# Kernel tuning notes

Hardware: AMD Instinct MI355X
Metric: run time of the kernel (lower is better)

The kernel has to match this reference:

```python
import jax, jax.numpy as jnp
import numpy as np

HIDDEN = 1024
MOE_INTER = 512
SHARED_INTER = 2048
N_EXPERTS = 32
TOP_K = 6
N_GROUP = 8
TOPK_GROUP = 4
ROUTED_SCALE = 2.5


def setup_inputs() -> dict:
    key = jax.random.key(0)
    ks = jax.random.split(key, 6)
    s = 0.02
    return {
        "hidden_states": jax.random.normal(ks[0], (2, 1024, HIDDEN), jnp.float32),
        "gate_w": jax.random.normal(ks[1], (N_EXPERTS, HIDDEN), jnp.float32) * s,
        "e_bias": jnp.zeros((N_EXPERTS,), jnp.float32),  # e_score_correction_bias (non-trainable)
        "up_w": jax.random.normal(ks[2], (N_EXPERTS, MOE_INTER, HIDDEN), jnp.float32) * s,
        "down_w": jax.random.normal(ks[3], (N_EXPERTS, HIDDEN, MOE_INTER), jnp.float32) * s,
        "shared_up_w": jax.random.normal(ks[4], (SHARED_INTER, HIDDEN), jnp.float32) * s,
        "shared_down_w": jax.random.normal(ks[5], (HIDDEN, SHARED_INTER), jnp.float32) * s,
    }


def _relu2(x):
    # Nemotron-H 'relu2' activation: relu(x)^2
    return jnp.square(jax.nn.relu(x))


def _router(x, gate_w, e_bias):
    # x: [T, H] -> topk_idx [T, K] (int), topk_w [T, K] (fp32)
    T = x.shape[0]
    logits = x.astype(jnp.float32) @ gate_w.astype(jnp.float32).T  # [T, E]
    scores = jax.nn.sigmoid(logits)
    sc = scores + e_bias[None, :]
    # group-limited routing: top-2 sum per group, keep topk_group groups
    g = sc.reshape(T, N_GROUP, N_EXPERTS // N_GROUP)
    group_scores = jax.lax.top_k(g, 2)[0].sum(-1)                  # [T, G]
    group_idx = jax.lax.top_k(group_scores, TOPK_GROUP)[1]         # [T, TG]
    group_mask = jnp.zeros_like(group_scores).at[jnp.arange(T)[:, None], group_idx].set(1.0)
    score_mask = jnp.repeat(group_mask, N_EXPERTS // N_GROUP, axis=1)  # [T, E]
    masked = jnp.where(score_mask > 0, sc, 0.0)
    topk_idx = jax.lax.stop_gradient(jax.lax.top_k(masked, TOP_K)[1])  # torch path is @no_grad
    topk_w = jnp.take_along_axis(scores, topk_idx, axis=1)         # gather from unbiased scores
    topk_w = topk_w / (topk_w.sum(-1, keepdims=True) + 1e-20)      # norm_topk_prob
    topk_w = topk_w * ROUTED_SCALE
    return topk_idx, topk_w


def reference(hidden_states, gate_w, e_bias, up_w, down_w, shared_up_w, shared_down_w):
    B, S, H = hidden_states.shape
    x = hidden_states.reshape(-1, H)  # [T, H]
    T = x.shape[0]
    topk_idx, topk_w = _router(x, gate_w, e_bias)
    # combine weights as dense [T, E] (scatter of top-k weights)
    combine = jnp.zeros((T, N_EXPERTS), topk_w.dtype).at[jnp.arange(T)[:, None], topk_idx].add(topk_w)
    # dense-masked expert compute; weight applied on intermediate (equivalent since
    # down_proj is linear with no bias): out = sum_e w_te * down_e(act(up_e(x)))
    h = _relu2(jnp.einsum('th,eih->tei', x, up_w))   # [T, E, I]
    h = h * combine[:, :, None]
    moe_out = jnp.einsum('tei,ehi->th', h, down_w)   # [T, H]
    shared = _relu2(x @ shared_up_w.T) @ shared_down_w.T
    return (moe_out + shared).reshape(B, S, H)


if __name__ == "__main__":
    out = reference(**setup_inputs())
    print(out.shape, out.dtype)
```

## Files before the change

### kernel.cpp

```cpp
#include <hip/hip_runtime.h>

typedef unsigned short u16;
typedef __bf16 bf16x8 __attribute__((ext_vector_type(8)));
typedef float f32x4 __attribute__((ext_vector_type(4)));
typedef u16 u16x8 __attribute__((ext_vector_type(8)));

#define T_TOK 2048
#define HID   1024
#define NEXP  32
#define IM    512
#define SI    2048
#define TOPK  6
#define PLAN_MAX 160

__device__ __forceinline__ u16 f2bf(float f){
  unsigned u = __float_as_uint(f);
  u += 0x7FFFu + ((u >> 16) & 1u);
  return (u16)(u >> 16);
}

__device__ __forceinline__ void gll16(const void* g, void* l){
  __builtin_amdgcn_global_load_lds((const __attribute__((address_space(1))) void*)g,
                                   (__attribute__((address_space(3))) void*)l, 16, 0, 0);
}

__device__ __forceinline__ u16x8 cvt2(float4 a, float4 b){
  u16x8 o;
  o[0] = f2bf(a.x); o[1] = f2bf(a.y); o[2] = f2bf(a.z); o[3] = f2bf(a.w);
  o[4] = f2bf(b.x); o[5] = f2bf(b.y); o[6] = f2bf(b.z); o[7] = f2bf(b.w);
  return o;
}

__global__ __launch_bounds__(256) void prep_kernel(
    const float* __restrict__ x, const float4* __restrict__ upw, const float4* __restrict__ dnw,
    const float4* __restrict__ supw, const float4* __restrict__ sdnw,
    const float* __restrict__ gate, const float* __restrict__ ebias,
    u16x8* __restrict__ xb, u16x8* __restrict__ upb, u16x8* __restrict__ dnb,
    u16x8* __restrict__ supb, u16x8* __restrict__ sdnb,
    int* __restrict__ ce, float* __restrict__ cw, int* __restrict__ done){
  int blk = blockIdx.x;
  if (blk == 0 && threadIdx.x == 0) *done = 0;
  if (blk >= 512){
    const float4* s; u16x8* d; long i;
    if (blk < 16896){
      i = (long)(blk - 512) * 256 + threadIdx.x;
      if (i < 2097152L){ s = upw; d = upb; }
      else             { s = dnw; d = dnb; i -= 2097152L; }
    } else {
      i = (long)(blk - 16896) * 256 + threadIdx.x;
      if      (i < 262144L){ s = (const float4*)x; d = xb; }
      else if (i < 524288L){ s = supw; d = supb; i -= 262144L; }
      else                 { s = sdnw; d = sdnb; i -= 524288L; }
    }
    float4 a = s[2*i], b = s[2*i+1];
    d[i] = cvt2(a, b);
    return;
  }
  int wave = threadIdx.x >> 6;
  int lane = threadIdx.x & 63;
  int t = blk * 4 + wave;
  int e = lane & 31, half = lane >> 5;
  const float4* xv = (const float4*)(x + (size_t)t * HID);
  const float4* gv = (const float4*)(gate + (size_t)e * HID);
  double d0a = 0, d1a = 0, d2a = 0, d3a = 0;
  for (int i = half * 128; i < half * 128 + 128; i++){
    float4 a = xv[i], b = gv[i];
    d0a += (double)a.x * b.x; d1a += (double)a.y * b.y;
    d2a += (double)a.z * b.z; d3a += (double)a.w * b.w;
  }
  double acc = (d0a + d1a) + (d2a + d3a);
  acc += __shfl_xor(acc, 32);
  double score = 1.0 / (1.0 + exp(-acc));
  double sc = score + (double)ebias[e];
  double o1  = __shfl_xor(sc, 1);
  double hi  = fmax(sc, o1), lo = fmin(sc, o1);
  double ohi = __shfl_xor(hi, 2), olo = __shfl_xor(lo, 2);
  double gs  = (hi >= ohi) ? hi + fmax(lo, ohi) : ohi + fmax(olo, hi);
  int g = e >> 2;
  int rank = 0;
#pragma unroll
  for (int j = 0; j < 8; j++){
    double gj = __shfl(gs, j * 4);
    if (gj > gs || (gj == gs && j < g)) rank++;
  }
  double cur = (rank < 4) ? sc : 0.0;
  int sel_e[TOPK]; double sel_w[TOPK]; double wsum = 0.0;
#pragma unroll
  for (int k = 0; k < TOPK; k++){
    double bv = cur; int bi = lane;
#pragma unroll
    for (int m = 32; m >= 1; m >>= 1){
      double ov = __shfl_xor(bv, m); int oi = __shfl_xor(bi, m);
      if (ov > bv || (ov == bv && oi < bi)) { bv = ov; bi = oi; }
    }
    if ((bi & 31) == e) cur = -1e300;
    double ws = __shfl(score, bi);
    sel_e[k] = bi; sel_w[k] = ws; wsum += ws;
  }
  double scale = 2.5 / (wsum + 1e-20);
#pragma unroll
  for (int k = 0; k < TOPK; k++){
    if (lane == k){
      ce[t * TOPK + k] = sel_e[k] & 31;
      cw[t * TOPK + k] = (float)(sel_w[k] * scale);
    }
  }
}

__global__ __launch_bounds__(256) void build_plan_kernel(const int* __restrict__ ce,
                                                         const float* __restrict__ cw,
                                                         int* __restrict__ cnt,
                                                         int* __restrict__ tok,
                                                         float* __restrict__ wl,
                                                         int* __restrict__ done,
                                                         int* __restrict__ plan){
  int e = blockIdx.x;
  int tid = threadIdx.x, lane = tid & 63, wave = tid >> 6;
  __shared__ int wsum[4];
  __shared__ int lastflag;
  int running = 0;
  for (int base = 0; base < T_TOK * TOPK; base += 256){
    int i = base + tid;
    bool m = (ce[i] == e);
    unsigned long long bal = __ballot(m);
    int woff = __popcll(bal & ((1ull << lane) - 1ull));
    if (lane == 0) wsum[wave] = __popcll(bal);
    __syncthreads();
    int wbase = 0;
#pragma unroll
    for (int wv = 0; wv < 4; wv++) if (wv < wave) wbase += wsum[wv];
    int btot = wsum[0] + wsum[1] + wsum[2] + wsum[3];
    if (m){
      int t = i / TOPK, k = i - t * TOPK;
      int pos = running + wbase + woff;
      tok[e * T_TOK + pos] = (t << 3) | k;
      wl[e * T_TOK + pos] = cw[i];
    }
    running += btot;
    __syncthreads();
  }
  if (tid == 0){
    atomicExch(&cnt[e], running);
    __threadfence();
    lastflag = (atomicAdd(done, 1) == NEXP - 1);
  }
  __syncthreads();
  if (lastflag){
    __threadfence();
    if (tid < PLAN_MAX) plan[1 + tid] = -1;
    __syncthreads();
    if (tid == 0){
      int n = 0;
      for (int ee = 0; ee < NEXP; ee++){
        int c = (ee == e) ? running : cnt[ee];
        for (int tb = 0; tb < c; tb += 128) plan[1 + n++] = (tb << 8) | ee;
      }
      plan[0] = n;
    }
  }
}

__device__ __forceinline__ void gemm_pipe(
    const char* gA0, const char* gA1, const char* gB0, const char* gB1,
    u16* lA, u16* lB, int iters, int tid, int wrow, int wcol, int qsw, int l16,
    f32x4 acc[4][4])
{
  char* bA = (char*)lA + tid*16;
  char* bB = (char*)lB + tid*16;
#define STAGE(t, b) do { \
    gll16(gA0 + (size_t)(t)*64, bA + (b)*8192); \
    gll16(gA1 + (size_t)(t)*64, bA + (b)*8192 + 4096); \
    gll16(gB0 + (size_t)(t)*64, bB + (b)*8192); \
    gll16(gB1 + (size_t)(t)*64, bB + (b)*8192 + 4096); } while(0)
#define COMPUTE(rbuf) do { \
    const u16* rA = lA + (rbuf)*4096; \
    const u16* rB = lB + (rbuf)*4096; \
    bf16x8 af[4], bfr[4]; \
    _Pragma("unroll") \
    for (int mt = 0; mt < 4; mt++) af[mt]  = *(const bf16x8*)&rA[(wrow + mt*16 + l16)*32 + qsw*8]; \
    _Pragma("unroll") \
    for (int nt = 0; nt < 4; nt++) bfr[nt] = *(const bf16x8*)&rB[(wcol + nt*16 + l16)*32 + qsw*8]; \
    _Pragma("unroll") \
    for (int mt = 0; mt < 4; mt++) \
    _Pragma("unroll") \
      for (int nt = 0; nt < 4; nt++) \
        acc[mt][nt] = __builtin_amdgcn_mfma_f32_16x16x32_bf16(af[mt], bfr[nt], acc[mt][nt], 0, 0, 0); \
    } while(0)

  STAGE(0, 0); STAGE(1, 1);
  int rb = 0, sb = 2;
  for (int it = 0; it < iters - 2; ++it){
    STAGE(it + 2, sb);
    asm volatile("s_waitcnt vmcnt(8)" ::: "memory");
    __builtin_amdgcn_s_barrier();
    asm volatile("" ::: "memory");
    COMPUTE(rb);
    asm volatile("" ::: "memory");
    __builtin_amdgcn_s_barrier();
    asm volatile("" ::: "memory");
    rb = (rb + 1 == 3) ? 0 : rb + 1;
    sb = (sb + 1 == 3) ? 0 : sb + 1;
  }
  asm volatile("s_waitcnt vmcnt(4)" ::: "memory");
  __builtin_amdgcn_s_barrier();
  asm volatile("" ::: "memory");
  COMPUTE(rb);
  asm volatile("" ::: "memory");
  __builtin_amdgcn_s_barrier();
  asm volatile("" ::: "memory");
  rb = (rb + 1 == 3) ? 0 : rb + 1;
  asm volatile("s_waitcnt vmcnt(0)" ::: "memory");
  __builtin_amdgcn_s_barrier();
  asm volatile("" ::: "memory");
  COMPUTE(rb);
#undef STAGE
#undef COMPUTE
}

#define ACC_INIT f32x4 acc[4][4]; \
  _Pragma("unroll") for (int i_ = 0; i_ < 4; i_++) \
  _Pragma("unroll") for (int j_ = 0; j_ < 4; j_++) acc[i_][j_] = (f32x4){0.f,0.f,0.f,0.f};

#define GEO_INIT int tid = threadIdx.x; \
  int lane = tid & 63, wave = tid >> 6, quad = lane >> 4, l16 = lane & 15; \
  int wrow = (wave >> 1)*64, wcol = (wave & 1)*64; \
  int srow = tid >> 2; \
  int sseg = ((tid & 3) ^ ((tid >> 3) & 3)) * 16; \
  int qsw  = quad ^ ((l16 >> 1) & 3);

__global__ __launch_bounds__(256) void up_fused_kernel(
    const u16* __restrict__ xb, const u16* __restrict__ supb, const u16* __restrict__ upb,
    const int* __restrict__ cnt, const int* __restrict__ tok, const float* __restrict__ wl,
    const int* __restrict__ plan, u16* __restrict__ shh, u16* __restrict__ hws){
  __shared__ u16 lA[3*4096], lB[3*4096];
  GEO_INIT;
  int blk = blockIdx.x;
  if (blk < 256){
    int bm = (blk >> 4) * 128, bn = (blk & 15) * 128;
    const char* gA0 = (const char*)(xb + (size_t)(bm + srow)*HID) + sseg;
    const char* gA1 = (const char*)(xb + (size_t)(bm + 64 + srow)*HID) + sseg;
    const char* gB0 = (const char*)(supb + (size_t)(bn + srow)*HID) + sseg;
    const char* gB1 = (const char*)(supb + (size_t)(bn + 64 + srow)*HID) + sseg;
    ACC_INIT;
    gemm_pipe(gA0, gA1, gB0, gB1, lA, lB, HID/32, tid, wrow, wcol, qsw, l16, acc);
#pragma unroll
    for (int mt = 0; mt < 4; mt++)
#pragma unroll
      for (int nt = 0; nt < 4; nt++)
#pragma unroll
        for (int r = 0; r < 4; r++){
          int m = bm + wrow + mt*16 + quad*4 + r;
          int n = bn + wcol + nt*16 + l16;
          float v = acc[mt][nt][r]; v = fmaxf(v, 0.f); v *= v;
          shh[(size_t)m*SI + n] = f2bf(v);
        }
  } else {
    int eu = blk - 256;
    int pv = plan[1 + (eu >> 2)];
    if (pv < 0) return;
    int e = pv & 255;
    int tb = pv >> 8;
    int c = cnt[e];
    int bn = (eu & 3) * 128;
    const int* tl = tok + e * T_TOK;
    const float* wle = wl + e * T_TOK;
    int s0 = tb + srow;      if (s0 > c-1) s0 = c-1;
    int s1 = tb + 64 + srow; if (s1 > c-1) s1 = c-1;
    int t0 = tl[s0] >> 3, t1 = tl[s1] >> 3;
    const char* gA0 = (const char*)(xb + (size_t)t0*HID) + sseg;
    const char* gA1 = (const char*)(xb + (size_t)t1*HID) + sseg;
    const u16* Bb = upb + (size_t)e * IM * HID;
    const char* gB0 = (const char*)(Bb + (size_t)(bn + srow)*HID) + sseg;
    const char* gB1 = (const char*)(Bb + (size_t)(bn + 64 + srow)*HID) + sseg;
    ACC_INIT;
    gemm_pipe(gA0, gA1, gB0, gB1, lA, lB, HID/32, tid, wrow, wcol, qsw, l16, acc);
#pragma unroll
    for (int mt = 0; mt < 4; mt++)
#pragma unroll
      for (int r = 0; r < 4; r++){
        int s = tb + wrow + mt*16 + quad*4 + r;
        if (s < c){
          int code = tl[s];
          float w = wle[s];
          size_t hb = ((size_t)(code >> 3) * TOPK + (code & 7)) * IM;
#pragma unroll
          for (int nt = 0; nt < 4; nt++){
            float v = acc[mt][nt][r]; v = fmaxf(v, 0.f); v = v * v * w;
            hws[hb + bn + wcol + nt*16 + l16] = f2bf(v);
          }
        }
      }
  }
}

__global__ __launch_bounds__(256) void down_fused_kernel(
    const u16* __restrict__ shh, const u16* __restrict__ sdnb,
    const u16* __restrict__ hws, const u16* __restrict__ dnb,
    const int* __restrict__ cnt, const int* __restrict__ tok, const int* __restrict__ plan,
    float* __restrict__ out){
  __shared__ u16 lA[3*4096], lB[3*4096];
  GEO_INIT;
  int blk = blockIdx.x;
  if (blk < 128){
    int bm = (blk >> 3)*128, bn = (blk & 7)*128;
    const char* gA0 = (const char*)(shh + (size_t)(bm + srow)*SI) + sseg;
    const char* gA1 = (const char*)(shh + (size_t)(bm + 64 + srow)*SI) + sseg;
    const char* gB0 = (const char*)(sdnb + (size_t)(bn + srow)*SI) + sseg;
    const char* gB1 = (const char*)(sdnb + (size_t)(bn + 64 + srow)*SI) + sseg;
    ACC_INIT;
    gemm_pipe(gA0, gA1, gB0, gB1, lA, lB, SI/32, tid, wrow, wcol, qsw, l16, acc);
#pragma unroll
    for (int mt = 0; mt < 4; mt++)
#pragma unroll
      for (int nt = 0; nt < 4; nt++)
#pragma unroll
        for (int r = 0; r < 4; r++){
          int m = bm + wrow + mt*16 + quad*4 + r;
          int n = bn + wcol + nt*16 + l16;
          unsafeAtomicAdd(&out[(size_t)m*HID + n], acc[mt][nt][r]);
        }
  } else {
    int eu = blk - 128;
    int pv = plan[1 + (eu >> 3)];
    if (pv < 0) return;
    int e = pv & 255;
    int tb = pv >> 8;
    int c = cnt[e];
    int bn = (eu & 7) * 128;
    const int* tl = tok + e * T_TOK;
    int s0 = tb + srow;      if (s0 > c-1) s0 = c-1;
    int s1 = tb + 64 + srow; if (s1 > c-1) s1 = c-1;
    int c0 = tl[s0], c1 = tl[s1];
    const char* gA0 = (const char*)(hws + ((size_t)(c0 >> 3)*TOPK + (c0 & 7))*IM) + sseg;
    const char* gA1 = (const char*)(hws + ((size_t)(c1 >> 3)*TOPK + (c1 & 7))*IM) + sseg;
    const u16* Bb = dnb + (size_t)e * HID * IM;
    const char* gB0 = (const char*)(Bb + (size_t)(bn + srow)*IM) + sseg;
    const char* gB1 = (const char*)(Bb + (size_t)(bn + 64 + srow)*IM) + sseg;
    ACC_INIT;
    gemm_pipe(gA0, gA1, gB0, gB1, lA, lB, IM/32, tid, wrow, wcol, qsw, l16, acc);
#pragma unroll
    for (int mt = 0; mt < 4; mt++)
#pragma unroll
      for (int r = 0; r < 4; r++){
        int s = tb + wrow + mt*16 + quad*4 + r;
        if (s < c){
          int code = tl[s];
          float* ob = out + (size_t)(code >> 3) * HID;
#pragma unroll
          for (int nt = 0; nt < 4; nt++)
            unsafeAtomicAdd(&ob[bn + wcol + nt*16 + l16], acc[mt][nt][r]);
        }
      }
  }
}

extern "C" void kernel_launch(void* const* d_in, const int* in_sizes, int n_in,
                              void* d_out, int out_size, void* d_ws, size_t ws_size,
                              hipStream_t stream) {
  const float* x    = (const float*)d_in[0];
  const float* gate = (const float*)d_in[1];
  const float* eb   = (const float*)d_in[2];
  const float* upw  = (const float*)d_in[3];
  const float* dnw  = (const float*)d_in[4];
  const float* supw = (const float*)d_in[5];
  const float* sdnw = (const float*)d_in[6];
  float* out = (float*)d_out;

  char* w = (char*)d_ws;
  size_t o = 0;
  int*   cnt  = (int*)(w + o);   o += 1024;
  int*   plan = (int*)(w + o);   o += 1024;
  int*   ce   = (int*)(w + o);   o += (size_t)T_TOK * TOPK * 4;
  float* cw   = (float*)(w + o); o += (size_t)T_TOK * TOPK * 4;
  int*   tok  = (int*)(w + o);   o += (size_t)NEXP * T_TOK * 4;
  float* wl   = (float*)(w + o); o += (size_t)NEXP * T_TOK * 4;
  u16*   xb   = (u16*)(w + o);   o += (size_t)T_TOK * HID * 2;
  u16*   dnb  = (u16*)(w + o);   o += (size_t)NEXP * HID * IM * 2;
  u16*   hws  = (u16*)(w + o);   o += (size_t)T_TOK * TOPK * IM * 2;
  u16*   upb  = (u16*)(w + o);   o += (size_t)NEXP * IM * HID * 2;
  u16*   supb = (u16*)(w + o);   o += (size_t)SI * HID * 2;
  u16*   sdnb = (u16*)(w + o);   o += (size_t)HID * SI * 2;
  u16*   shh  = (u16*)(w + o);   o += (size_t)T_TOK * SI * 2;
  int*   done = cnt + 32;

  hipMemsetAsync(out, 0, (size_t)T_TOK * HID * 4, stream);
  prep_kernel<<<19968, 256, 0, stream>>>(
      x, (const float4*)upw, (const float4*)dnw, (const float4*)supw, (const float4*)sdnw,
      gate, eb, (u16x8*)xb, (u16x8*)upb, (u16x8*)dnb, (u16x8*)supb, (u16x8*)sdnb,
      ce, cw, done);
  build_plan_kernel<<<NEXP, 256, 0, stream>>>(ce, cw, cnt, tok, wl, done, plan);
  up_fused_kernel<<<896, 256, 0, stream>>>(xb, supb, upb, cnt, tok, wl, plan, shh, hws);
  down_fused_kernel<<<1408, 256, 0, stream>>>(shh, sdnb, hws, dnb, cnt, tok, plan, out);
}
```

Before: 335.7 us.

## Spread fp32-to-bf16 weight conversions across later kernels and split shared down GEMM along K

```diff
diff --git a/kernel.cpp b/kernel.cpp
--- a/kernel.cpp
+++ b/kernel.cpp
@@ -31,29 +31,20 @@
   return o;
 }
 
-__global__ __launch_bounds__(256) void prep_kernel(
-    const float* __restrict__ x, const float4* __restrict__ upw, const float4* __restrict__ dnw,
-    const float4* __restrict__ supw, const float4* __restrict__ sdnw,
+__device__ __forceinline__ void cvt_blk(const float4* __restrict__ s, u16x8* __restrict__ d, long i){
+  float4 a = s[2*i], b = s[2*i+1];
+  d[i] = cvt2(a, b);
+}
+
+__global__ __launch_bounds__(256) void prep1_kernel(
+    const float* __restrict__ x, const float4* __restrict__ upw,
     const float* __restrict__ gate, const float* __restrict__ ebias,
-    u16x8* __restrict__ xb, u16x8* __restrict__ upb, u16x8* __restrict__ dnb,
-    u16x8* __restrict__ supb, u16x8* __restrict__ sdnb,
-    int* __restrict__ ce, float* __restrict__ cw, int* __restrict__ done){
+    u16x8* __restrict__ upb, int* __restrict__ ce, float* __restrict__ cw,
+    int* __restrict__ done){
   int blk = blockIdx.x;
   if (blk == 0 && threadIdx.x == 0) *done = 0;
   if (blk >= 512){
-    const float4* s; u16x8* d; long i;
-    if (blk < 16896){
-      i = (long)(blk - 512) * 256 + threadIdx.x;
-      if (i < 2097152L){ s = upw; d = upb; }
-      else             { s = dnw; d = dnb; i -= 2097152L; }
-    } else {
-      i = (long)(blk - 16896) * 256 + threadIdx.x;
-      if      (i < 262144L){ s = (const float4*)x; d = xb; }
-      else if (i < 524288L){ s = supw; d = supb; i -= 262144L; }
-      else                 { s = sdnw; d = sdnb; i -= 524288L; }
-    }
-    float4 a = s[2*i], b = s[2*i+1];
-    d[i] = cvt2(a, b);
+    cvt_blk(upw, upb, (long)(blk - 512) * 256 + threadIdx.x);
     return;
   }
   int wave = threadIdx.x >> 6;
@@ -107,14 +98,20 @@
   }
 }
 
-__global__ __launch_bounds__(256) void build_plan_kernel(const int* __restrict__ ce,
-                                                         const float* __restrict__ cw,
-                                                         int* __restrict__ cnt,
-                                                         int* __restrict__ tok,
-                                                         float* __restrict__ wl,
-                                                         int* __restrict__ done,
-                                                         int* __restrict__ plan){
-  int e = blockIdx.x;
+__global__ __launch_bounds__(256) void build_plan_cvt_kernel(
+    const int* __restrict__ ce, const float* __restrict__ cw,
+    int* __restrict__ cnt, int* __restrict__ tok, float* __restrict__ wl,
+    int* __restrict__ done, int* __restrict__ plan,
+    const float4* __restrict__ x, const float4* __restrict__ supw,
+    u16x8* __restrict__ xb, u16x8* __restrict__ supb){
+  int blk = blockIdx.x;
+  if (blk >= 32){
+    long i = (long)(blk - 32) * 256 + threadIdx.x;
+    if (i < 262144L) cvt_blk(x, xb, i);
+    else             cvt_blk(supw, supb, i - 262144L);
+    return;
+  }
+  int e = blk;
   int tid = threadIdx.x, lane = tid & 63, wave = tid >> 6;
   __shared__ int wsum[4];
   __shared__ int lastflag;
@@ -231,10 +228,18 @@
 __global__ __launch_bounds__(256) void up_fused_kernel(
     const u16* __restrict__ xb, const u16* __restrict__ supb, const u16* __restrict__ upb,
     const int* __restrict__ cnt, const int* __restrict__ tok, const float* __restrict__ wl,
-    const int* __restrict__ plan, u16* __restrict__ shh, u16* __restrict__ hws){
+    const int* __restrict__ plan, u16* __restrict__ shh, u16* __restrict__ hws,
+    const float4* __restrict__ dnw, const float4* __restrict__ sdnw,
+    u16x8* __restrict__ dnb, u16x8* __restrict__ sdnb){
+  int blk = blockIdx.x;
+  if (blk >= 896){
+    long i = (long)(blk - 896) * 256 + threadIdx.x;
+    if (i < 2097152L) cvt_blk(dnw, dnb, i);
+    else              cvt_blk(sdnw, sdnb, i - 2097152L);
+    return;
+  }
   __shared__ u16 lA[3*4096], lB[3*4096];
   GEO_INIT;
-  int blk = blockIdx.x;
   if (blk < 256){
     int bm = (blk >> 4) * 128, bn = (blk & 15) * 128;
     const char* gA0 = (const char*)(xb + (size_t)(bm + srow)*HID) + sseg;
@@ -301,14 +306,16 @@
   __shared__ u16 lA[3*4096], lB[3*4096];
   GEO_INIT;
   int blk = blockIdx.x;
-  if (blk < 128){
-    int bm = (blk >> 3)*128, bn = (blk & 7)*128;
-    const char* gA0 = (const char*)(shh + (size_t)(bm + srow)*SI) + sseg;
-    const char* gA1 = (const char*)(shh + (size_t)(bm + 64 + srow)*SI) + sseg;
-    const char* gB0 = (const char*)(sdnb + (size_t)(bn + srow)*SI) + sseg;
-    const char* gB1 = (const char*)(sdnb + (size_t)(bn + 64 + srow)*SI) + sseg;
+  if (blk < 256){
+    int kc = blk & 1;
+    int t  = blk >> 1;
+    int bm = (t >> 3)*128, bn = (t & 7)*128;
+    const char* gA0 = (const char*)(shh + (size_t)(bm + srow)*SI + kc*1024) + sseg;
+    const char* gA1 = (const char*)(shh + (size_t)(bm + 64 + srow)*SI + kc*1024) + sseg;
+    const char* gB0 = (const char*)(sdnb + (size_t)(bn + srow)*SI + kc*1024) + sseg;
+    const char* gB1 = (const char*)(sdnb + (size_t)(bn + 64 + srow)*SI + kc*1024) + sseg;
     ACC_INIT;
-    gemm_pipe(gA0, gA1, gB0, gB1, lA, lB, SI/32, tid, wrow, wcol, qsw, l16, acc);
+    gemm_pipe(gA0, gA1, gB0, gB1, lA, lB, 32, tid, wrow, wcol, qsw, l16, acc);
 #pragma unroll
     for (int mt = 0; mt < 4; mt++)
 #pragma unroll
@@ -320,7 +327,7 @@
           unsafeAtomicAdd(&out[(size_t)m*HID + n], acc[mt][nt][r]);
         }
   } else {
-    int eu = blk - 128;
+    int eu = blk - 256;
     int pv = plan[1 + (eu >> 3)];
     if (pv < 0) return;
     int e = pv & 255;
@@ -384,11 +391,13 @@
   int*   done = cnt + 32;
 
   hipMemsetAsync(out, 0, (size_t)T_TOK * HID * 4, stream);
-  prep_kernel<<<19968, 256, 0, stream>>>(
-      x, (const float4*)upw, (const float4*)dnw, (const float4*)supw, (const float4*)sdnw,
-      gate, eb, (u16x8*)xb, (u16x8*)upb, (u16x8*)dnb, (u16x8*)supb, (u16x8*)sdnb,
-      ce, cw, done);
-  build_plan_kernel<<<NEXP, 256, 0, stream>>>(ce, cw, cnt, tok, wl, done, plan);
-  up_fused_kernel<<<896, 256, 0, stream>>>(xb, supb, upb, cnt, tok, wl, plan, shh, hws);
-  down_fused_kernel<<<1408, 256, 0, stream>>>(shh, sdnb, hws, dnb, cnt, tok, plan, out);
-}
+  prep1_kernel<<<8704, 256, 0, stream>>>(
+      x, (const float4*)upw, gate, eb, (u16x8*)upb, ce, cw, done);
+  build_plan_cvt_kernel<<<2080, 256, 0, stream>>>(
+      ce, cw, cnt, tok, wl, done, plan,
+      (const float4*)x, (const float4*)supw, (u16x8*)xb, (u16x8*)supb);
+  up_fused_kernel<<<10112, 256, 0, stream>>>(
+      xb, supb, upb, cnt, tok, wl, plan, shh, hws,
+      (const float4*)dnw, (const float4*)sdnw, (u16x8*)dnb, (u16x8*)sdnb);
+  down_fused_kernel<<<1536, 256, 0, stream>>>(shh, sdnb, hws, dnb, cnt, tok, plan, out);
+}
```

Result: slower. 348.5 us (+3.8%).

## Fuse fp32-to-bf16 weight conversion into GEMM B-operand loads

Applied to the files above, without the earlier changes.

```diff
diff --git a/kernel.cpp b/kernel.cpp
--- a/kernel.cpp
+++ b/kernel.cpp
@@ -31,29 +31,17 @@
   return o;
 }
 
-__global__ __launch_bounds__(256) void prep_kernel(
-    const float* __restrict__ x, const float4* __restrict__ upw, const float4* __restrict__ dnw,
-    const float4* __restrict__ supw, const float4* __restrict__ sdnw,
-    const float* __restrict__ gate, const float* __restrict__ ebias,
-    u16x8* __restrict__ xb, u16x8* __restrict__ upb, u16x8* __restrict__ dnb,
-    u16x8* __restrict__ supb, u16x8* __restrict__ sdnb,
+__global__ __launch_bounds__(256) void prep1_kernel(
+    const float* __restrict__ x, const float* __restrict__ gate,
+    const float* __restrict__ ebias, u16x8* __restrict__ xb,
     int* __restrict__ ce, float* __restrict__ cw, int* __restrict__ done){
   int blk = blockIdx.x;
   if (blk == 0 && threadIdx.x == 0) *done = 0;
   if (blk >= 512){
-    const float4* s; u16x8* d; long i;
-    if (blk < 16896){
-      i = (long)(blk - 512) * 256 + threadIdx.x;
-      if (i < 2097152L){ s = upw; d = upb; }
-      else             { s = dnw; d = dnb; i -= 2097152L; }
-    } else {
-      i = (long)(blk - 16896) * 256 + threadIdx.x;
-      if      (i < 262144L){ s = (const float4*)x; d = xb; }
-      else if (i < 524288L){ s = supw; d = supb; i -= 262144L; }
-      else                 { s = sdnw; d = sdnb; i -= 524288L; }
-    }
+    long i = (long)(blk - 512) * 256 + threadIdx.x;
+    const float4* s = (const float4*)x;
     float4 a = s[2*i], b = s[2*i+1];
-    d[i] = cvt2(a, b);
+    xb[i] = cvt2(a, b);
     return;
   }
   int wave = threadIdx.x >> 6;
@@ -161,17 +149,24 @@
 }
 
 __device__ __forceinline__ void gemm_pipe(
-    const char* gA0, const char* gA1, const char* gB0, const char* gB1,
+    const char* gA0, const char* gA1, const char* gB0f, const char* gB1f,
     u16* lA, u16* lB, int iters, int tid, int wrow, int wcol, int qsw, int l16,
     f32x4 acc[4][4])
 {
-  char* bA = (char*)lA + tid*16;
-  char* bB = (char*)lB + tid*16;
-#define STAGE(t, b) do { \
-    gll16(gA0 + (size_t)(t)*64, bA + (b)*8192); \
-    gll16(gA1 + (size_t)(t)*64, bA + (b)*8192 + 4096); \
-    gll16(gB0 + (size_t)(t)*64, bB + (b)*8192); \
-    gll16(gB1 + (size_t)(t)*64, bB + (b)*8192 + 4096); } while(0)
+  char* bA  = (char*)lA + tid*16;
+  char* bBw = (char*)lB + tid*16;
+  float4 p0a, p0b, p0c, p0d, p1a, p1b, p1c, p1d;
+#define ASTAGE(t, b) do { \
+    gll16(gA0 + (size_t)(t)*64, bA + (size_t)(b)*8192); \
+    gll16(gA1 + (size_t)(t)*64, bA + (size_t)(b)*8192 + 4096); } while(0)
+#define BLOAD(t, Pa, Pb, Pc, Pd) do { \
+    Pa = *(const float4*)(gB0f + (size_t)(t)*128); \
+    Pb = *(const float4*)(gB0f + (size_t)(t)*128 + 16); \
+    Pc = *(const float4*)(gB1f + (size_t)(t)*128); \
+    Pd = *(const float4*)(gB1f + (size_t)(t)*128 + 16); } while(0)
+#define BWRITE(Pa, Pb, Pc, Pd, b) do { \
+    *(u16x8*)(bBw + (size_t)(b)*8192)        = cvt2(Pa, Pb); \
+    *(u16x8*)(bBw + (size_t)(b)*8192 + 4096) = cvt2(Pc, Pd); } while(0)
 #define COMPUTE(rbuf) do { \
     const u16* rA = lA + (rbuf)*4096; \
     const u16* rB = lB + (rbuf)*4096; \
@@ -187,33 +182,60 @@
         acc[mt][nt] = __builtin_amdgcn_mfma_f32_16x16x32_bf16(af[mt], bfr[nt], acc[mt][nt], 0, 0, 0); \
     } while(0)
 
-  STAGE(0, 0); STAGE(1, 1);
-  int rb = 0, sb = 2;
-  for (int it = 0; it < iters - 2; ++it){
-    STAGE(it + 2, sb);
-    asm volatile("s_waitcnt vmcnt(8)" ::: "memory");
+  ASTAGE(0, 0); BLOAD(0, p0a, p0b, p0c, p0d);
+  ASTAGE(1, 1); BLOAD(1, p1a, p1b, p1c, p1d);
+  asm volatile("s_waitcnt vmcnt(6)" ::: "memory");
+  BWRITE(p0a, p0b, p0c, p0d, 0);
+  int rb = 0;
+  for (int t = 0; t <= iters - 4; t += 2){
+    {
+      int b2 = rb + 2; if (b2 >= 3) b2 -= 3;
+      ASTAGE(t + 2, b2); BLOAD(t + 2, p0a, p0b, p0c, p0d);
+      asm volatile("s_waitcnt vmcnt(6)" ::: "memory");
+      int b1 = rb + 1; if (b1 >= 3) b1 -= 3;
+      BWRITE(p1a, p1b, p1c, p1d, b1);
+      asm volatile("s_waitcnt lgkmcnt(0)" ::: "memory");
+      __builtin_amdgcn_s_barrier();
+      asm volatile("" ::: "memory");
+      COMPUTE(rb);
+      asm volatile("" ::: "memory");
+      __builtin_amdgcn_s_barrier();
+      asm volatile("" ::: "memory");
+      rb = b1;
+    }
+    {
+      int b2 = rb + 2; if (b2 >= 3) b2 -= 3;
+      ASTAGE(t + 3, b2); BLOAD(t + 3, p1a, p1b, p1c, p1d);
+      asm volatile("s_waitcnt vmcnt(6)" ::: "memory");
+      int b1 = rb + 1; if (b1 >= 3) b1 -= 3;
+      BWRITE(p0a, p0b, p0c, p0d, b1);
+      asm volatile("s_waitcnt lgkmcnt(0)" ::: "memory");
+      __builtin_amdgcn_s_barrier();
+      asm volatile("" ::: "memory");
+      COMPUTE(rb);
+      asm volatile("" ::: "memory");
+      __builtin_amdgcn_s_barrier();
+      asm volatile("" ::: "memory");
+      rb = b1;
+    }
+  }
+  asm volatile("s_waitcnt vmcnt(0)" ::: "memory");
+  {
+    int b1 = rb + 1; if (b1 >= 3) b1 -= 3;
+    BWRITE(p1a, p1b, p1c, p1d, b1);
+    asm volatile("s_waitcnt lgkmcnt(0)" ::: "memory");
     __builtin_amdgcn_s_barrier();
     asm volatile("" ::: "memory");
     COMPUTE(rb);
     asm volatile("" ::: "memory");
     __builtin_amdgcn_s_barrier();
     asm volatile("" ::: "memory");
-    rb = (rb + 1 == 3) ? 0 : rb + 1;
-    sb = (sb + 1 == 3) ? 0 : sb + 1;
-  }
-  asm volatile("s_waitcnt vmcnt(4)" ::: "memory");
-  __builtin_amdgcn_s_barrier();
-  asm volatile("" ::: "memory");
+    rb = b1;
+  }
   COMPUTE(rb);
-  asm volatile("" ::: "memory");
-  __builtin_amdgcn_s_barrier();
-  asm volatile("" ::: "memory");
-  rb = (rb + 1 == 3) ? 0 : rb + 1;
-  asm volatile("s_waitcnt vmcnt(0)" ::: "memory");
-  __builtin_amdgcn_s_barrier();
-  asm volatile("" ::: "memory");
-  COMPUTE(rb);
-#undef STAGE
+#undef ASTAGE
+#undef BLOAD
+#undef BWRITE
 #undef COMPUTE
 }
 
@@ -229,7 +251,7 @@
   int qsw  = quad ^ ((l16 >> 1) & 3);
 
 __global__ __launch_bounds__(256) void up_fused_kernel(
-    const u16* __restrict__ xb, const u16* __restrict__ supb, const u16* __restrict__ upb,
+    const u16* __restrict__ xb, const float* __restrict__ supw, const float* __restrict__ upw,
     const int* __restrict__ cnt, const int* __restrict__ tok, const float* __restrict__ wl,
     const int* __restrict__ plan, u16* __restrict__ shh, u16* __restrict__ hws){
   __shared__ u16 lA[3*4096], lB[3*4096];
@@ -239,8 +261,8 @@
     int bm = (blk >> 4) * 128, bn = (blk & 15) * 128;
     const char* gA0 = (const char*)(xb + (size_t)(bm + srow)*HID) + sseg;
     const char* gA1 = (const char*)(xb + (size_t)(bm + 64 + srow)*HID) + sseg;
-    const char* gB0 = (const char*)(supb + (size_t)(bn + srow)*HID) + sseg;
-    const char* gB1 = (const char*)(supb + (size_t)(bn + 64 + srow)*HID) + sseg;
+    const char* gB0 = (const char*)supw + (size_t)(bn + srow)*HID*4 + sseg*2;
+    const char* gB1 = (const char*)supw + (size_t)(bn + 64 + srow)*HID*4 + sseg*2;
     ACC_INIT;
     gemm_pipe(gA0, gA1, gB0, gB1, lA, lB, HID/32, tid, wrow, wcol, qsw, l16, acc);
 #pragma unroll
@@ -269,9 +291,9 @@
     int t0 = tl[s0] >> 3, t1 = tl[s1] >> 3;
     const char* gA0 = (const char*)(xb + (size_t)t0*HID) + sseg;
     const char* gA1 = (const char*)(xb + (size_t)t1*HID) + sseg;
-    const u16* Bb = upb + (size_t)e * IM * HID;
-    const char* gB0 = (const char*)(Bb + (size_t)(bn + srow)*HID) + sseg;
-    const char* gB1 = (const char*)(Bb + (size_t)(bn + 64 + srow)*HID) + sseg;
+    const float* Bb = upw + (size_t)e * IM * HID;
+    const char* gB0 = (const char*)Bb + (size_t)(bn + srow)*HID*4 + sseg*2;
+    const char* gB1 = (const char*)Bb + (size_t)(bn + 64 + srow)*HID*4 + sseg*2;
     ACC_INIT;
     gemm_pipe(gA0, gA1, gB0, gB1, lA, lB, HID/32, tid, wrow, wcol, qsw, l16, acc);
 #pragma unroll
@@ -294,8 +316,8 @@
 }
 
 __global__ __launch_bounds__(256) void down_fused_kernel(
-    const u16* __restrict__ shh, const u16* __restrict__ sdnb,
-    const u16* __restrict__ hws, const u16* __restrict__ dnb,
+    const u16* __restrict__ shh, const float* __restrict__ sdnw,
+    const u16* __restrict__ hws, const float* __restrict__ dnw,
     const int* __restrict__ cnt, const int* __restrict__ tok, const int* __restrict__ plan,
     float* __restrict__ out){
   __shared__ u16 lA[3*4096], lB[3*4096];
@@ -305,8 +327,8 @@
     int bm = (blk >> 3)*128, bn = (blk & 7)*128;
     const char* gA0 = (const char*)(shh + (size_t)(bm + srow)*SI) + sseg;
     const char* gA1 = (const char*)(shh + (size_t)(bm + 64 + srow)*SI) + sseg;
-    const char* gB0 = (const char*)(sdnb + (size_t)(bn + srow)*SI) + sseg;
-    const char* gB1 = (const char*)(sdnb + (size_t)(bn + 64 + srow)*SI) + sseg;
+    const char* gB0 = (const char*)sdnw + (size_t)(bn + srow)*SI*4 + sseg*2;
+    const char* gB1 = (const char*)sdnw + (size_t)(bn + 64 + srow)*SI*4 + sseg*2;
     ACC_INIT;
     gemm_pipe(gA0, gA1, gB0, gB1, lA, lB, SI/32, tid, wrow, wcol, qsw, l16, acc);
 #pragma unroll
@@ -333,9 +355,9 @@
     int c0 = tl[s0], c1 = tl[s1];
     const char* gA0 = (const char*)(hws + ((size_t)(c0 >> 3)*TOPK + (c0 & 7))*IM) + sseg;
     const char* gA1 = (const char*)(hws + ((size_t)(c1 >> 3)*TOPK + (c1 & 7))*IM) + sseg;
-    const u16* Bb = dnb + (size_t)e * HID * IM;
-    const char* gB0 = (const char*)(Bb + (size_t)(bn + srow)*IM) + sseg;
-    const char* gB1 = (const char*)(Bb + (size_t)(bn + 64 + srow)*IM) + sseg;
+    const float* Bb = dnw + (size_t)e * HID * IM;
+    const char* gB0 = (const char*)Bb + (size_t)(bn + srow)*IM*4 + sseg*2;
+    const char* gB1 = (const char*)Bb + (size_t)(bn + 64 + srow)*IM*4 + sseg*2;
     ACC_INIT;
     gemm_pipe(gA0, gA1, gB0, gB1, lA, lB, IM/32, tid, wrow, wcol, qsw, l16, acc);
 #pragma unroll
@@ -375,20 +397,13 @@
   int*   tok  = (int*)(w + o);   o += (size_t)NEXP * T_TOK * 4;
   float* wl   = (float*)(w + o); o += (size_t)NEXP * T_TOK * 4;
   u16*   xb   = (u16*)(w + o);   o += (size_t)T_TOK * HID * 2;
-  u16*   dnb  = (u16*)(w + o);   o += (size_t)NEXP * HID * IM * 2;
   u16*   hws  = (u16*)(w + o);   o += (size_t)T_TOK * TOPK * IM * 2;
-  u16*   upb  = (u16*)(w + o);   o += (size_t)NEXP * IM * HID * 2;
-  u16*   supb = (u16*)(w + o);   o += (size_t)SI * HID * 2;
-  u16*   sdnb = (u16*)(w + o);   o += (size_t)HID * SI * 2;
   u16*   shh  = (u16*)(w + o);   o += (size_t)T_TOK * SI * 2;
   int*   done = cnt + 32;
 
-  hipMemsetAsync(out, 0, (size_t)T_TOK * HID * 4, stream);
-  prep_kernel<<<19968, 256, 0, stream>>>(
-      x, (const float4*)upw, (const float4*)dnw, (const float4*)supw, (const float4*)sdnw,
-      gate, eb, (u16x8*)xb, (u16x8*)upb, (u16x8*)dnb, (u16x8*)supb, (u16x8*)sdnb,
-      ce, cw, done);
+  (void)hipMemsetAsync(out, 0, (size_t)T_TOK * HID * 4, stream);
+  prep1_kernel<<<1536, 256, 0, stream>>>(x, gate, eb, (u16x8*)xb, ce, cw, done);
   build_plan_kernel<<<NEXP, 256, 0, stream>>>(ce, cw, cnt, tok, wl, done, plan);
-  up_fused_kernel<<<896, 256, 0, stream>>>(xb, supb, upb, cnt, tok, wl, plan, shh, hws);
-  down_fused_kernel<<<1408, 256, 0, stream>>>(shh, sdnb, hws, dnb, cnt, tok, plan, out);
-}
+  up_fused_kernel<<<896, 256, 0, stream>>>(xb, supw, upw, cnt, tok, wl, plan, shh, hws);
+  down_fused_kernel<<<1408, 256, 0, stream>>>(shh, sdnw, hws, dnw, cnt, tok, plan, out);
+}
```

New measurement: 395.9 us. 17.9% more time.
